# Performance work log

Measured on AMD Instinct MI355X. Metric: run time of the kernel, lower is better.

The kernel has to match this reference:

```python
import jax, jax.numpy as jnp
import numpy as np
import math

N = 50000      # nodes (single node type 'mapping_var')
D = 128        # in_feats
R = 3          # relations
E = 800000     # edges per relation
OUT = 64
ALPHA = 0.5
BETA1 = math.log(2.0)    # log(lambda/layer + 1), layer=1, lambda=1
BETA2 = math.log(1.5)    # layer=2
SLOPE = 0.01             # leaky_relu default negative slope


def setup_inputs() -> dict:
    key = jax.random.key(0)
    ks = jax.random.split(key, 8)
    x = jax.random.normal(ks[0], (N, D), dtype=jnp.float32)
    src = jax.random.randint(ks[1], (R, E), 0, N, dtype=jnp.int32)
    dst = jax.random.randint(ks[2], (R, E), 0, N, dtype=jnp.int32)
    W1 = jax.random.normal(ks[3], (R, D, D), dtype=jnp.float32) * 0.05
    b1 = jnp.zeros((R, D), dtype=jnp.float32)
    W2 = jax.random.normal(ks[4], (R, D, D), dtype=jnp.float32) * 0.05
    b2 = jnp.zeros((R, D), dtype=jnp.float32)
    Wlin = jax.random.normal(ks[5], (D, OUT), dtype=jnp.float32) * 0.05
    blin = jnp.zeros((OUT,), dtype=jnp.float32)
    return {"x": x, "src": src, "dst": dst, "W1": W1, "b1": b1,
            "W2": W2, "b2": b2, "Wlin": Wlin, "blin": blin}


def _gcn2_rel(h, feat0, src, dst, W, b, beta, act):
    """One GCN2Conv on one relation. h,feat0: [N,D]; src,dst: [E]."""
    ones = jnp.ones(src.shape, h.dtype)
    deg_out = jnp.maximum(jax.ops.segment_sum(ones, src, num_segments=N), 1.0)
    deg_in = jnp.maximum(jax.ops.segment_sum(ones, dst, num_segments=N), 1.0)
    hs = h * (deg_out ** -0.5)[:, None]              # src-side normalize
    agg = jax.ops.segment_sum(hs[src], dst, num_segments=N)  # SpMM via gather+scatter
    feat = agg * (deg_in ** -0.5)[:, None]           # dst-side normalize
    rst = feat * (1.0 - ALPHA) + ALPHA * feat0       # initial-residual blend
    rst = (1.0 - beta) * rst + beta * (rst @ W) + b  # identity mapping (project_initial_features)
    if act:
        rst = jnp.where(rst >= 0, rst, SLOPE * rst)  # leaky_relu
    return rst


def reference(x, src, dst, W1, b1, W2, b2, Wlin, blin):
    # conv1: per-relation GCN2Conv(layer=1, leaky_relu), mean-aggregate over relations
    h1 = jax.vmap(lambda s, d, w, bb: _gcn2_rel(x, x, s, d, w, bb, BETA1, True))(
        src, dst, W1, b1).mean(axis=0)
    # dropout: eval-mode identity
    # conv2: per-relation GCN2Conv(layer=2, no activation), feat_0 = original inputs
    h2 = jax.vmap(lambda s, d, w, bb: _gcn2_rel(h1, x, s, d, w, bb, BETA2, False))(
        src, dst, W2, b2).mean(axis=0)
    return h2 @ Wlin + blin
```

## Files before the change

kernel.cpp:

```cpp
#include <hip/hip_runtime.h>

#define NN    50000
#define DD    128
#define RR    3
#define EE    800000
#define OUTD  64
#define BKT   128
#define NBK   391
#define CAP   2560
#define CAPB  2560
#define CHUNK 8192
#define NCH   98
#define NPB   3125
#define SETUPB 6250
#define ALPHA_ 0.5f
#define SLOPE_ 0.01f
#define BETA1_ 0.6931471805599453f
#define BETA2_ 0.4054651081081644f

typedef __attribute__((ext_vector_type(8))) short short8;
typedef __attribute__((ext_vector_type(4))) float f32x4;

__device__ __forceinline__ unsigned short f2b(float f) {
    unsigned int u = __builtin_bit_cast(unsigned int, f);
    u += 0x7FFFu + ((u >> 16) & 1u);
    return (unsigned short)(u >> 16);
}
__device__ __forceinline__ unsigned int pack2(float lo, float hi) {
    return (unsigned int)f2b(lo) | ((unsigned int)f2b(hi) << 16);
}
__device__ __forceinline__ float blo(unsigned int w) { return __builtin_bit_cast(float, w << 16); }
__device__ __forceinline__ float bhi(unsigned int w) { return __builtin_bit_cast(float, w & 0xFFFF0000u); }

__global__ __launch_bounds__(256) void bin_kernel(
    const int* __restrict__ src, const int* __restrict__ dst,
    int* __restrict__ bcnt_d, int* __restrict__ bcnt_s,
    int* __restrict__ pairs_d, unsigned short* __restrict__ pairs_s)
{
    __shared__ int hist[NBK];
    __shared__ int lbase[NBK];
    __shared__ int gdelta[NBK];
    __shared__ int lcur[NBK];
    __shared__ unsigned int staging[CHUNK];
    unsigned short* staging16 = (unsigned short*)staging;
    const int tid = threadIdx.x;
    const int blk = blockIdx.x;
    const int phase = (blk >= RR * NCH);
    const int rb = phase ? blk - RR * NCH : blk;
    const int r = rb / NCH;
    const int chunk = rb % NCH;
    const int e0 = chunk * CHUNK;
    const int n = min(CHUNK, EE - e0);
    const int* sp = src + (size_t)r * EE + e0;
    const int* dp = dst + (size_t)r * EE + e0;
    const int* kp = phase ? sp : dp;

    for (int i = tid; i < NBK; i += 256) hist[i] = 0;
    __syncthreads();
    for (int i = tid; i < n; i += 256)
        atomicAdd(&hist[kp[i] >> 7], 1);
    __syncthreads();
    if (tid < 64) {
        int carry = 0;
        for (int c0 = 0; c0 < NBK; c0 += 64) {
            const int idx = c0 + tid;
            const int v = (idx < NBK) ? hist[idx] : 0;
            int incl = v;
            #pragma unroll
            for (int d = 1; d < 64; d <<= 1) {
                const int t = __shfl_up(incl, d, 64);
                if (tid >= d) incl += t;
            }
            if (idx < NBK) lbase[idx] = carry + incl - v;
            carry += __shfl(incl, 63, 64);
        }
    }
    __syncthreads();
    if (!phase) {
        for (int b = tid; b < NBK; b += 256) {
            lcur[b] = lbase[b];
            const int h = hist[b];
            if (h > 0) {
                const int gstart = (r * NBK + b) * CAP + atomicAdd(&bcnt_d[r * NBK + b], h);
                gdelta[b] = gstart - lbase[b];
            }
        }
        __syncthreads();
        for (int i = tid; i < n; i += 256) {
            const int d = dp[i];
            const int b = d >> 7;
            const int pos = atomicAdd(&lcur[b], 1);
            staging[pos] = (unsigned int)sp[i] | ((unsigned int)(d & 127) << 16)
                         | ((unsigned int)b << 23);
        }
        __syncthreads();
        for (int j = tid; j < n; j += 256) {
            const unsigned int v = staging[j];
            const int b = v >> 23;
            const int gi = gdelta[b] + j;
            const int lo = gi - (r * NBK + b) * CAP;
            if (lo < CAP) pairs_d[gi] = (int)(v & 0x7FFFFF);
        }
    } else {
        for (int b = tid; b < NBK; b += 256) {
            lcur[b] = lbase[b];
            const int h = hist[b];
            if (h > 0) {
                const int gstart = (r * NBK + b) * CAPB + atomicAdd(&bcnt_s[r * NBK + b], h);
                gdelta[b] = gstart - lbase[b];
            }
        }
        __syncthreads();
        for (int i = tid; i < n; i += 256) {
            const int s = sp[i];
            const int b = s >> 7;
            const int pos = atomicAdd(&lcur[b], 1);
            staging16[pos] = (unsigned short)((b << 7) | (s & 127));
        }
        __syncthreads();
        for (int j = tid; j < n; j += 256) {
            const unsigned short v = staging16[j];
            const int b = v >> 7;
            const int gi = gdelta[b] + j;
            const int lo = gi - (r * NBK + b) * CAPB;
            if (lo < CAPB) pairs_s[gi] = v;
        }
    }
}

__global__ __launch_bounds__(256) void dego_setup_kernel(
    const unsigned short* __restrict__ pairs_s, const int* __restrict__ bcnt_s,
    float* __restrict__ dego_r,
    const float* __restrict__ x, unsigned short* __restrict__ xb,
    const float* __restrict__ W1, const float* __restrict__ W2,
    const float* __restrict__ Wlin, unsigned short* __restrict__ Wt1,
    unsigned short* __restrict__ Wt2, unsigned short* __restrict__ WlT)
{
    __shared__ int scnt[BKT];
    const int tid = threadIdx.x;
    const int blk = blockIdx.x;
    if (blk < RR * NBK) {
        const int n2 = min(bcnt_s[blk], CAPB);
        const unsigned short* ps = pairs_s + (size_t)blk * CAPB;
        if (tid < BKT) scnt[tid] = 0;
        __syncthreads();
        for (int i = tid; i < n2; i += 256)
            atomicAdd(&scnt[ps[i] & 127], 1);
        __syncthreads();
        if (tid < BKT) {
            const int r = blk / NBK;
            const int g = (blk % NBK) * BKT + tid;
            if (g < NN)
                dego_r[r * NN + g] = rsqrtf((float)max(scnt[tid], 1));
        }
    } else {
        const int i = (blk - RR * NBK) * 256 + tid;
        {
            const float4 v = ((const float4*)x)[i];
            ushort4 o;
            o.x = f2b(v.x); o.y = f2b(v.y); o.z = f2b(v.z); o.w = f2b(v.w);
            ((ushort4*)xb)[i] = o;
        }
        if (i < RR * DD * DD) {
            const int r = i >> 14, rem = i & 16383, nn = rem >> 7, k = rem & 127;
            const float diag = (k == nn) ? 1.0f : 0.0f;
            const float w1 = W1[r * DD * DD + k * DD + nn];
            Wt1[i] = f2b(BETA1_ * w1 + diag * (1.0f - BETA1_));
            const float w2 = W2[r * DD * DD + k * DD + nn];
            Wt2[i] = f2b((BETA2_ * w2 + diag * (1.0f - BETA2_)) * (1.0f / 3.0f));
        } else if (i < RR * DD * DD + OUTD * DD) {
            const int j = i - RR * DD * DD;
            const int nn = j >> 7, k = j & 127;
            WlT[j] = f2b(Wlin[k * OUTD + nn]);
        }
    }
}

__global__ __launch_bounds__(256) void sort_kernel(
    int* __restrict__ pairs_d, const int* __restrict__ bcnt_d,
    const float* __restrict__ dego_r,
    int* __restrict__ off_g, int* __restrict__ cnt_g, float* __restrict__ degi_r)
{
    __shared__ int stage[CAP];
    __shared__ int cnt[BKT];
    __shared__ int base[BKT];
    __shared__ int pos[BKT];
    const int tid = threadIdx.x;
    const int bid = blockIdx.x;
    const int rr = bid / NBK;
    const int n = min(bcnt_d[bid], CAP);
    int* pp = pairs_d + (size_t)bid * CAP;
    const float* dego = dego_r + (size_t)rr * NN;
    if (tid < BKT) cnt[tid] = 0;
    __syncthreads();
    for (int i = tid; i < n; i += 256) {
        const int p = pp[i];
        stage[i] = p;
        atomicAdd(&cnt[p >> 16], 1);
    }
    __syncthreads();
    if (tid < 64) {
        int carry = 0;
        for (int c0 = 0; c0 < BKT; c0 += 64) {
            const int v = cnt[c0 + tid];
            int incl = v;
            #pragma unroll
            for (int d = 1; d < 64; d <<= 1) {
                const int t = __shfl_up(incl, d, 64);
                if (tid >= d) incl += t;
            }
            base[c0 + tid] = carry + incl - v;
            carry += __shfl(incl, 63, 64);
        }
    }
    __syncthreads();
    if (tid < BKT) {
        pos[tid] = base[tid];
        const int g = (bid % NBK) * BKT + tid;
        if (g < NN) {
            off_g[rr * NN + g] = bid * CAP + base[tid];
            cnt_g[rr * NN + g] = cnt[tid];
            degi_r[rr * NN + g] = rsqrtf((float)max(cnt[tid], 1));
        }
    }
    __syncthreads();
    for (int i = tid; i < n; i += 256) {
        const int p = stage[i];
        const int q = atomicAdd(&pos[p >> 16], 1);
        const int s = p & 0xFFFF;
        pp[q] = s | ((int)f2b(dego[s]) << 16);
    }
}

__global__ __launch_bounds__(256) void pull_all_kernel(
    const unsigned short* __restrict__ hb,
    const unsigned short* __restrict__ xb,
    const int* __restrict__ csrw, const int* __restrict__ off_g,
    const int* __restrict__ cnt_g, const float* __restrict__ degi_r,
    unsigned short* __restrict__ aggb)
{
    const int blk = blockIdx.x;
    const int r = blk / NPB;
    const int node = (blk % NPB) * 16 + (threadIdx.x >> 4);
    const int lane = threadIdx.x & 15;
    const int gi = r * NN + node;
    const int j0 = off_g[gi];
    const int j1 = j0 + cnt_g[gi];
    const uint4* hb4 = (const uint4*)hb;
    float a0 = 0.f, a1 = 0.f, a2 = 0.f, a3 = 0.f, a4 = 0.f, a5 = 0.f, a6 = 0.f, a7 = 0.f;
    int j = j0;
    for (; j + 4 <= j1; j += 4) {
        const unsigned int p0 = csrw[j],     p1 = csrw[j + 1];
        const unsigned int p2 = csrw[j + 2], p3 = csrw[j + 3];
        const float n0 = bhi(p0), n1 = bhi(p1), n2 = bhi(p2), n3 = bhi(p3);
        const uint4 q0 = hb4[(size_t)(p0 & 0xFFFF) * 16 + lane];
        const uint4 q1 = hb4[(size_t)(p1 & 0xFFFF) * 16 + lane];
        const uint4 q2 = hb4[(size_t)(p2 & 0xFFFF) * 16 + lane];
        const uint4 q3 = hb4[(size_t)(p3 & 0xFFFF) * 16 + lane];
        a0 += blo(q0.x) * n0 + blo(q1.x) * n1 + blo(q2.x) * n2 + blo(q3.x) * n3;
        a1 += bhi(q0.x) * n0 + bhi(q1.x) * n1 + bhi(q2.x) * n2 + bhi(q3.x) * n3;
        a2 += blo(q0.y) * n0 + blo(q1.y) * n1 + blo(q2.y) * n2 + blo(q3.y) * n3;
        a3 += bhi(q0.y) * n0 + bhi(q1.y) * n1 + bhi(q2.y) * n2 + bhi(q3.y) * n3;
        a4 += blo(q0.z) * n0 + blo(q1.z) * n1 + blo(q2.z) * n2 + blo(q3.z) * n3;
        a5 += bhi(q0.z) * n0 + bhi(q1.z) * n1 + bhi(q2.z) * n2 + bhi(q3.z) * n3;
        a6 += blo(q0.w) * n0 + blo(q1.w) * n1 + blo(q2.w) * n2 + blo(q3.w) * n3;
        a7 += bhi(q0.w) * n0 + bhi(q1.w) * n1 + bhi(q2.w) * n2 + bhi(q3.w) * n3;
    }
    for (; j < j1; ++j) {
        const unsigned int p0 = csrw[j];
        const float n0 = bhi(p0);
        const uint4 q0 = hb4[(size_t)(p0 & 0xFFFF) * 16 + lane];
        a0 += blo(q0.x) * n0; a1 += bhi(q0.x) * n0;
        a2 += blo(q0.y) * n0; a3 += bhi(q0.y) * n0;
        a4 += blo(q0.z) * n0; a5 += bhi(q0.z) * n0;
        a6 += blo(q0.w) * n0; a7 += bhi(q0.w) * n0;
    }
    const float nd = degi_r[gi] * (1.0f - ALPHA_);
    const uint4 xq = ((const uint4*)xb)[(size_t)node * 16 + lane];
    uint4 o;
    o.x = pack2(a0 * nd + ALPHA_ * blo(xq.x), a1 * nd + ALPHA_ * bhi(xq.x));
    o.y = pack2(a2 * nd + ALPHA_ * blo(xq.y), a3 * nd + ALPHA_ * bhi(xq.y));
    o.z = pack2(a4 * nd + ALPHA_ * blo(xq.z), a5 * nd + ALPHA_ * bhi(xq.z));
    o.w = pack2(a6 * nd + ALPHA_ * blo(xq.w), a7 * nd + ALPHA_ * bhi(xq.w));
    ((uint4*)aggb)[(size_t)gi * 16 + lane] = o;
}

template<int LIN>
__global__ __launch_bounds__(256) void conv_mfma_kernel(
    const unsigned short* __restrict__ aggb,
    const unsigned short* __restrict__ WtG,
    const float* __restrict__ bias,
    const unsigned short* __restrict__ WlT,
    const float* __restrict__ blin,
    unsigned short* __restrict__ houtb,
    float* __restrict__ outf)
{
    __shared__ unsigned short WtL[DD * 136];
    uint4* WtL4 = (uint4*)WtL;
    const int tid  = threadIdx.x;
    const int wave = tid >> 6;
    const int lane = tid & 63;
    const int l15  = lane & 15;
    const int q    = lane >> 4;
    const int blockRow = blockIdx.x * 64;
    const int row0 = blockRow + wave * 16;
    const int arow = min(row0 + l15, NN - 1);

    f32x4 o[8];
    if (LIN) {
        #pragma unroll
        for (int ct = 0; ct < 8; ++ct) {
            const int col = ct * 16 + l15;
            const float bv = (bias[col] + bias[DD + col] + bias[2 * DD + col]) * (1.0f / 3.0f);
            o[ct] = (f32x4){bv, bv, bv, bv};
        }
    } else {
        #pragma unroll
        for (int ct = 0; ct < 8; ++ct) o[ct] = (f32x4){0.f, 0.f, 0.f, 0.f};
    }

    short8 a_cur[4], a_nxt[4];
    {
        const uint4* ap = (const uint4*)aggb + (size_t)arow * 16 + q;
        #pragma unroll
        for (int ks = 0; ks < 4; ++ks)
            a_cur[ks] = __builtin_bit_cast(short8, ap[ks * 4]);
    }

    for (int r = 0; r < RR; ++r) {
        __syncthreads();
        const uint4* wg = (const uint4*)(WtG + (size_t)r * DD * DD);
        for (int i = tid; i < DD * 16; i += 256)
            WtL4[(i >> 4) * 17 + (i & 15)] = wg[i];
        if (r + 1 < RR) {
            const uint4* ap = (const uint4*)aggb + ((size_t)(r + 1) * NN + arow) * 16 + q;
            #pragma unroll
            for (int ks = 0; ks < 4; ++ks)
                a_nxt[ks] = __builtin_bit_cast(short8, ap[ks * 4]);
        }
        __syncthreads();

        #pragma unroll
        for (int ct = 0; ct < 8; ++ct) {
            f32x4 acc;
            if (LIN) {
                acc = o[ct];
            } else {
                const float bv = bias[r * DD + ct * 16 + l15];
                acc = (f32x4){bv, bv, bv, bv};
            }
            const int nrow = ct * 16 + l15;
            #pragma unroll
            for (int ks = 0; ks < 4; ++ks) {
                const short8 b = __builtin_bit_cast(short8, WtL4[nrow * 17 + ks * 4 + q]);
                acc = __builtin_amdgcn_mfma_f32_16x16x32_bf16(a_cur[ks], b, acc, 0, 0, 0);
            }
            if (LIN) {
                o[ct] = acc;
            } else {
                #pragma unroll
                for (int e = 0; e < 4; ++e) {
                    float v = acc[e];
                    v = v >= 0.f ? v : SLOPE_ * v;
                    o[ct][e] += v * (1.0f / 3.0f);
                }
            }
        }
        #pragma unroll
        for (int ks = 0; ks < 4; ++ks) a_cur[ks] = a_nxt[ks];
    }

    __syncthreads();
    unsigned short* tile = WtL;
    #pragma unroll
    for (int ct = 0; ct < 8; ++ct) {
        const int col = ct * 16 + l15;
        #pragma unroll
        for (int e = 0; e < 4; ++e) {
            const int lrow = wave * 16 + q * 4 + e;
            tile[lrow * 136 + col] = f2b(o[ct][e]);
        }
    }
    if (LIN) {
        uint4* wl4 = WtL4 + 64 * 17;
        const uint4* wg = (const uint4*)WlT;
        for (int i = tid; i < OUTD * 16; i += 256)
            wl4[(i >> 4) * 17 + (i & 15)] = wg[i];
    }
    __syncthreads();

    if (!LIN) {
        for (int i = tid; i < 64 * 16; i += 256) {
            const int lrow = i >> 4, c = i & 15;
            const int grow = blockRow + lrow;
            if (grow < NN)
                ((uint4*)houtb)[(size_t)grow * 16 + c] = WtL4[lrow * 17 + c];
        }
    } else {
        short8 a2[4];
        const int lrow = wave * 16 + l15;
        #pragma unroll
        for (int ks = 0; ks < 4; ++ks)
            a2[ks] = __builtin_bit_cast(short8, WtL4[lrow * 17 + ks * 4 + q]);
        #pragma unroll
        for (int ct = 0; ct < 4; ++ct) {
            const int col = ct * 16 + l15;
            const float bv = blin[col];
            f32x4 acc = (f32x4){bv, bv, bv, bv};
            #pragma unroll
            for (int ks = 0; ks < 4; ++ks) {
                const short8 b = __builtin_bit_cast(short8, WtL4[(64 + col) * 17 + ks * 4 + q]);
                acc = __builtin_amdgcn_mfma_f32_16x16x32_bf16(a2[ks], b, acc, 0, 0, 0);
            }
            #pragma unroll
            for (int e = 0; e < 4; ++e) {
                const int grow = row0 + q * 4 + e;
                if (grow < NN) outf[(size_t)grow * OUTD + col] = acc[e];
            }
        }
    }
}

extern "C" void kernel_launch(void* const* d_in, const int* in_sizes, int n_in,
                              void* d_out, int out_size, void* d_ws, size_t ws_size,
                              hipStream_t stream)
{
    const float* x    = (const float*)d_in[0];
    const int*   src  = (const int*)  d_in[1];
    const int*   dst  = (const int*)  d_in[2];
    const float* W1   = (const float*)d_in[3];
    const float* b1   = (const float*)d_in[4];
    const float* W2   = (const float*)d_in[5];
    const float* b2   = (const float*)d_in[6];
    const float* Wlin = (const float*)d_in[7];
    const float* blin = (const float*)d_in[8];
    float* out = (float*)d_out;

    int*   bcnt_d  = (int*)d_ws;
    int*   bcnt_s  = bcnt_d + RR * NBK;
    float* dego_r  = (float*)(bcnt_s + RR * NBK);
    float* degi_r  = dego_r + RR * NN;
    int*   off_g   = (int*)(degi_r + RR * NN);
    int*   cnt_g   = off_g + RR * NN;
    int*   pairs_d = cnt_g + RR * NN + 2;
    unsigned short* pairs_s = (unsigned short*)(pairs_d + (size_t)RR * NBK * CAP);
    unsigned short* xb   = pairs_s + (size_t)RR * NBK * CAPB;
    unsigned short* h1b  = xb + (size_t)NN * DD;
    unsigned short* aggb = h1b + (size_t)NN * DD;
    unsigned short* Wt1  = aggb + (size_t)RR * NN * DD;
    unsigned short* Wt2  = Wt1 + RR * DD * DD;
    unsigned short* WlT  = Wt2 + RR * DD * DD;

    hipMemsetAsync(bcnt_d, 0, (size_t)2 * RR * NBK * sizeof(int), stream);

    const int gemm_blocks = (NN + 63) / 64;

    bin_kernel<<<2 * RR * NCH, 256, 0, stream>>>(src, dst, bcnt_d, bcnt_s, pairs_d, pairs_s);
    dego_setup_kernel<<<RR * NBK + SETUPB, 256, 0, stream>>>(
        pairs_s, bcnt_s, dego_r, x, xb, W1, W2, Wlin, Wt1, Wt2, WlT);
    sort_kernel<<<RR * NBK, 256, 0, stream>>>(
        pairs_d, bcnt_d, dego_r, off_g, cnt_g, degi_r);

    pull_all_kernel<<<RR * NPB, 256, 0, stream>>>(
        xb, xb, pairs_d, off_g, cnt_g, degi_r, aggb);
    conv_mfma_kernel<0><<<gemm_blocks, 256, 0, stream>>>(
        aggb, Wt1, b1, nullptr, nullptr, h1b, nullptr);

    pull_all_kernel<<<RR * NPB, 256, 0, stream>>>(
        h1b, xb, pairs_d, off_g, cnt_g, degi_r, aggb);
    conv_mfma_kernel<1><<<gemm_blocks, 256, 0, stream>>>(
        aggb, Wt2, b2, WlT, blin, nullptr, out);
}
```

Baseline: 405.7 us.

## Fold layer-2 projection and final linear into pre-aggregation 64-wide GEMM

Layer 2 had no activation, so its per-relation identity mapping, the relation mean and the final linear are folded into combined matrices M_r = (beta*W2_r + (1-beta)I)·Wlin/3, plus a constant bias vector. These are built in the setup kernel. A new GEMM projects h1 (and x for the residual term) to 64 columns before aggregation, and a 64-wide pull kernel then gathers and sums over the three relations straight into the output. This halves the gathered bytes in the second SpMM and removes the 128x128 second conv GEMM, at the cost of an extra bf16 rounding of the projected features and a small serial matmul in setup.

```diff
diff --git a/kernel.cpp b/kernel.cpp
--- a/kernel.cpp
+++ b/kernel.cpp
@@ -13,6 +13,9 @@
 #define NCH   98
 #define NPB   3125
 #define SETUPB 6250
+#define MCB   49
+#define PGB   391
+#define P64B  3125
 #define ALPHA_ 0.5f
 #define SLOPE_ 0.01f
 #define BETA1_ 0.6931471805599453f
@@ -20,6 +23,7 @@
 
 typedef __attribute__((ext_vector_type(8))) short short8;
 typedef __attribute__((ext_vector_type(4))) float f32x4;
+typedef __attribute__((ext_vector_type(4))) unsigned int u32x4;
 
 __device__ __forceinline__ unsigned short f2b(float f) {
     unsigned int u = __builtin_bit_cast(unsigned int, f);
@@ -134,7 +138,9 @@
     const float* __restrict__ x, unsigned short* __restrict__ xb,
     const float* __restrict__ W1, const float* __restrict__ W2,
     const float* __restrict__ Wlin, unsigned short* __restrict__ Wt1,
-    unsigned short* __restrict__ Wt2, unsigned short* __restrict__ WlT)
+    unsigned short* __restrict__ Wt2, unsigned short* __restrict__ WlT,
+    const float* __restrict__ b2, const float* __restrict__ blin,
+    unsigned short* __restrict__ MT, float* __restrict__ Cbuf)
 {
     __shared__ int scnt[BKT];
     const int tid = threadIdx.x;
@@ -153,7 +159,7 @@
             if (g < NN)
                 dego_r[r * NN + g] = rsqrtf((float)max(scnt[tid], 1));
         }
-    } else {
+    } else if (blk < RR * NBK + SETUPB) {
         const int i = (blk - RR * NBK) * 256 + tid;
         {
             const float4 v = ((const float4*)x)[i];
@@ -173,6 +179,31 @@
             const int nn = j >> 7, k = j & 127;
             WlT[j] = f2b(Wlin[k * OUTD + nn]);
         }
+    } else {
+        const int mb = blk - RR * NBK - SETUPB;
+        if (mb < MCB - 1) {
+            const int base = (mb * 256 + tid) * 2;
+            #pragma unroll
+            for (int ii = 0; ii < 2; ++ii) {
+                const int gidx = base + ii;
+                const int r = gidx >> 13;
+                const int rem = gidx & 8191;
+                const int o = rem >> 7, k = rem & 127;
+                float s = 0.f;
+                for (int nn = 0; nn < DD; ++nn)
+                    s += W2[r * DD * DD + k * DD + nn] * Wlin[nn * OUTD + o];
+                MT[gidx] = f2b((BETA2_ / 3.0f) * s + ((1.0f - BETA2_) / 3.0f) * Wlin[k * OUTD + o]);
+            }
+        } else {
+            if (tid < OUTD) {
+                float s = blin[tid];
+                for (int nn = 0; nn < DD; ++nn) {
+                    const float mb2 = (b2[nn] + b2[DD + nn] + b2[2 * DD + nn]) * (1.0f / 3.0f);
+                    s += mb2 * Wlin[nn * OUTD + tid];
+                }
+                Cbuf[tid] = s;
+            }
+        }
     }
 }
 
@@ -246,17 +277,17 @@
     const int gi = r * NN + node;
     const int j0 = off_g[gi];
     const int j1 = j0 + cnt_g[gi];
-    const uint4* hb4 = (const uint4*)hb;
+    const u32x4* hb4 = (const u32x4*)hb;
     float a0 = 0.f, a1 = 0.f, a2 = 0.f, a3 = 0.f, a4 = 0.f, a5 = 0.f, a6 = 0.f, a7 = 0.f;
     int j = j0;
     for (; j + 4 <= j1; j += 4) {
         const unsigned int p0 = csrw[j],     p1 = csrw[j + 1];
         const unsigned int p2 = csrw[j + 2], p3 = csrw[j + 3];
         const float n0 = bhi(p0), n1 = bhi(p1), n2 = bhi(p2), n3 = bhi(p3);
-        const uint4 q0 = hb4[(size_t)(p0 & 0xFFFF) * 16 + lane];
-        const uint4 q1 = hb4[(size_t)(p1 & 0xFFFF) * 16 + lane];
-        const uint4 q2 = hb4[(size_t)(p2 & 0xFFFF) * 16 + lane];
-        const uint4 q3 = hb4[(size_t)(p3 & 0xFFFF) * 16 + lane];
+        const u32x4 q0 = hb4[(size_t)(p0 & 0xFFFF) * 16 + lane];
+        const u32x4 q1 = hb4[(size_t)(p1 & 0xFFFF) * 16 + lane];
+        const u32x4 q2 = hb4[(size_t)(p2 & 0xFFFF) * 16 + lane];
+        const u32x4 q3 = hb4[(size_t)(p3 & 0xFFFF) * 16 + lane];
         a0 += blo(q0.x) * n0 + blo(q1.x) * n1 + blo(q2.x) * n2 + blo(q3.x) * n3;
         a1 += bhi(q0.x) * n0 + bhi(q1.x) * n1 + bhi(q2.x) * n2 + bhi(q3.x) * n3;
         a2 += blo(q0.y) * n0 + blo(q1.y) * n1 + blo(q2.y) * n2 + blo(q3.y) * n3;
@@ -269,20 +300,20 @@
     for (; j < j1; ++j) {
         const unsigned int p0 = csrw[j];
         const float n0 = bhi(p0);
-        const uint4 q0 = hb4[(size_t)(p0 & 0xFFFF) * 16 + lane];
+        const u32x4 q0 = hb4[(size_t)(p0 & 0xFFFF) * 16 + lane];
         a0 += blo(q0.x) * n0; a1 += bhi(q0.x) * n0;
         a2 += blo(q0.y) * n0; a3 += bhi(q0.y) * n0;
         a4 += blo(q0.z) * n0; a5 += bhi(q0.z) * n0;
         a6 += blo(q0.w) * n0; a7 += bhi(q0.w) * n0;
     }
     const float nd = degi_r[gi] * (1.0f - ALPHA_);
-    const uint4 xq = ((const uint4*)xb)[(size_t)node * 16 + lane];
-    uint4 o;
+    const u32x4 xq = ((const u32x4*)xb)[(size_t)node * 16 + lane];
+    u32x4 o;
     o.x = pack2(a0 * nd + ALPHA_ * blo(xq.x), a1 * nd + ALPHA_ * bhi(xq.x));
     o.y = pack2(a2 * nd + ALPHA_ * blo(xq.y), a3 * nd + ALPHA_ * bhi(xq.y));
     o.z = pack2(a4 * nd + ALPHA_ * blo(xq.z), a5 * nd + ALPHA_ * bhi(xq.z));
     o.w = pack2(a6 * nd + ALPHA_ * blo(xq.w), a7 * nd + ALPHA_ * bhi(xq.w));
-    ((uint4*)aggb)[(size_t)gi * 16 + lane] = o;
+    ((u32x4*)aggb)[(size_t)gi * 16 + lane] = o;
 }
 
 template<int LIN>
@@ -381,44 +412,138 @@
             tile[lrow * 136 + col] = f2b(o[ct][e]);
         }
     }
-    if (LIN) {
-        uint4* wl4 = WtL4 + 64 * 17;
-        const uint4* wg = (const uint4*)WlT;
-        for (int i = tid; i < OUTD * 16; i += 256)
-            wl4[(i >> 4) * 17 + (i & 15)] = wg[i];
-    }
-    __syncthreads();
-
-    if (!LIN) {
-        for (int i = tid; i < 64 * 16; i += 256) {
-            const int lrow = i >> 4, c = i & 15;
-            const int grow = blockRow + lrow;
-            if (grow < NN)
-                ((uint4*)houtb)[(size_t)grow * 16 + c] = WtL4[lrow * 17 + c];
-        }
-    } else {
-        short8 a2[4];
-        const int lrow = wave * 16 + l15;
-        #pragma unroll
-        for (int ks = 0; ks < 4; ++ks)
-            a2[ks] = __builtin_bit_cast(short8, WtL4[lrow * 17 + ks * 4 + q]);
+    __syncthreads();
+    for (int i = tid; i < 64 * 16; i += 256) {
+        const int lrow = i >> 4, c = i & 15;
+        const int grow = blockRow + lrow;
+        if (grow < NN)
+            ((uint4*)houtb)[(size_t)grow * 16 + c] = WtL4[lrow * 17 + c];
+    }
+}
+
+__global__ __launch_bounds__(512) void pgemm_kernel(
+    const unsigned short* __restrict__ h1b,
+    const unsigned short* __restrict__ xb,
+    const unsigned short* __restrict__ MT,
+    unsigned short* __restrict__ Pb,
+    unsigned short* __restrict__ Qb)
+{
+    __shared__ unsigned short MTL[RR * 64 * 136];
+    uint4* MTL4 = (uint4*)MTL;
+    const int tid  = threadIdx.x;
+    const int wave = tid >> 6;
+    const int lane = tid & 63;
+    const int l15  = lane & 15;
+    const int q    = lane >> 4;
+    const int blockRow = blockIdx.x * 128;
+    const int row0 = blockRow + wave * 16;
+    const int arow = min(row0 + l15, NN - 1);
+
+    {
+        const uint4* mg = (const uint4*)MT;
+        for (int i = tid; i < RR * 64 * 16; i += 512)
+            MTL4[(i >> 4) * 17 + (i & 15)] = mg[i];
+    }
+    short8 ah[4], ax[4];
+    {
+        const uint4* hp = (const uint4*)h1b + (size_t)arow * 16 + q;
+        const uint4* xp = (const uint4*)xb + (size_t)arow * 16 + q;
+        #pragma unroll
+        for (int ks = 0; ks < 4; ++ks) {
+            ah[ks] = __builtin_bit_cast(short8, hp[ks * 4]);
+            ax[ks] = __builtin_bit_cast(short8, xp[ks * 4]);
+        }
+    }
+    __syncthreads();
+
+    for (int r = 0; r < RR; ++r) {
         #pragma unroll
         for (int ct = 0; ct < 4; ++ct) {
-            const int col = ct * 16 + l15;
-            const float bv = blin[col];
-            f32x4 acc = (f32x4){bv, bv, bv, bv};
+            f32x4 acc = (f32x4){0.f, 0.f, 0.f, 0.f};
+            const int orow = r * 64 + ct * 16 + l15;
             #pragma unroll
             for (int ks = 0; ks < 4; ++ks) {
-                const short8 b = __builtin_bit_cast(short8, WtL4[(64 + col) * 17 + ks * 4 + q]);
-                acc = __builtin_amdgcn_mfma_f32_16x16x32_bf16(a2[ks], b, acc, 0, 0, 0);
+                const short8 b = __builtin_bit_cast(short8, MTL4[orow * 17 + ks * 4 + q]);
+                acc = __builtin_amdgcn_mfma_f32_16x16x32_bf16(ah[ks], b, acc, 0, 0, 0);
             }
             #pragma unroll
             for (int e = 0; e < 4; ++e) {
                 const int grow = row0 + q * 4 + e;
-                if (grow < NN) outf[(size_t)grow * OUTD + col] = acc[e];
-            }
-        }
-    }
+                if (grow < NN)
+                    Pb[((size_t)r * NN + grow) * OUTD + ct * 16 + l15] = f2b(acc[e]);
+            }
+        }
+    }
+    #pragma unroll
+    for (int ct = 0; ct < 4; ++ct) {
+        f32x4 acc = (f32x4){0.f, 0.f, 0.f, 0.f};
+        for (int r = 0; r < RR; ++r) {
+            const int orow = r * 64 + ct * 16 + l15;
+            #pragma unroll
+            for (int ks = 0; ks < 4; ++ks) {
+                const short8 b = __builtin_bit_cast(short8, MTL4[orow * 17 + ks * 4 + q]);
+                acc = __builtin_amdgcn_mfma_f32_16x16x32_bf16(ax[ks], b, acc, 0, 0, 0);
+            }
+        }
+        #pragma unroll
+        for (int e = 0; e < 4; ++e) {
+            const int grow = row0 + q * 4 + e;
+            if (grow < NN)
+                Qb[(size_t)grow * OUTD + ct * 16 + l15] = f2b(acc[e] * ALPHA_);
+        }
+    }
+}
+
+__global__ __launch_bounds__(256) void pull64_kernel(
+    const unsigned short* __restrict__ Pb,
+    const unsigned short* __restrict__ Qb,
+    const float* __restrict__ Cbuf,
+    const int* __restrict__ csrw, const int* __restrict__ off_g,
+    const int* __restrict__ cnt_g, const float* __restrict__ degi_r,
+    float* __restrict__ outf)
+{
+    const int node = blockIdx.x * 16 + (threadIdx.x >> 4);
+    const int lane = threadIdx.x & 15;
+    const uint2* P2 = (const uint2*)Pb;
+    float t0, t1, t2, t3;
+    {
+        const uint2 qq = ((const uint2*)Qb)[(size_t)node * 16 + lane];
+        const float4 cv = ((const float4*)Cbuf)[lane];
+        t0 = blo(qq.x) + cv.x; t1 = bhi(qq.x) + cv.y;
+        t2 = blo(qq.y) + cv.z; t3 = bhi(qq.y) + cv.w;
+    }
+    for (int r = 0; r < RR; ++r) {
+        const int gi = r * NN + node;
+        const int j0 = off_g[gi];
+        const int j1 = j0 + cnt_g[gi];
+        const uint2* Pr = P2 + (size_t)r * NN * 16;
+        float a0 = 0.f, a1 = 0.f, a2 = 0.f, a3 = 0.f;
+        int j = j0;
+        for (; j + 4 <= j1; j += 4) {
+            const unsigned int p0 = csrw[j],     p1 = csrw[j + 1];
+            const unsigned int p2 = csrw[j + 2], p3 = csrw[j + 3];
+            const float n0 = bhi(p0), n1 = bhi(p1), n2 = bhi(p2), n3 = bhi(p3);
+            const uint2 q0 = Pr[(size_t)(p0 & 0xFFFF) * 16 + lane];
+            const uint2 q1 = Pr[(size_t)(p1 & 0xFFFF) * 16 + lane];
+            const uint2 q2 = Pr[(size_t)(p2 & 0xFFFF) * 16 + lane];
+            const uint2 q3 = Pr[(size_t)(p3 & 0xFFFF) * 16 + lane];
+            a0 += blo(q0.x) * n0 + blo(q1.x) * n1 + blo(q2.x) * n2 + blo(q3.x) * n3;
+            a1 += bhi(q0.x) * n0 + bhi(q1.x) * n1 + bhi(q2.x) * n2 + bhi(q3.x) * n3;
+            a2 += blo(q0.y) * n0 + blo(q1.y) * n1 + blo(q2.y) * n2 + blo(q3.y) * n3;
+            a3 += bhi(q0.y) * n0 + bhi(q1.y) * n1 + bhi(q2.y) * n2 + bhi(q3.y) * n3;
+        }
+        for (; j < j1; ++j) {
+            const unsigned int p0 = csrw[j];
+            const float n0 = bhi(p0);
+            const uint2 q0 = Pr[(size_t)(p0 & 0xFFFF) * 16 + lane];
+            a0 += blo(q0.x) * n0; a1 += bhi(q0.x) * n0;
+            a2 += blo(q0.y) * n0; a3 += bhi(q0.y) * n0;
+        }
+        const float nd = degi_r[gi] * (1.0f - ALPHA_);
+        t0 += a0 * nd; t1 += a1 * nd; t2 += a2 * nd; t3 += a3 * nd;
+    }
+    float4 ov; ov.x = t0; ov.y = t1; ov.z = t2; ov.w = t3;
+    ((float4*)outf)[(size_t)node * 16 + lane] = ov;
 }
 
 extern "C" void kernel_launch(void* const* d_in, const int* in_sizes, int n_in,
@@ -450,14 +575,18 @@
     unsigned short* Wt1  = aggb + (size_t)RR * NN * DD;
     unsigned short* Wt2  = Wt1 + RR * DD * DD;
     unsigned short* WlT  = Wt2 + RR * DD * DD;
+    unsigned short* MT   = WlT + OUTD * DD;
+    float*          Cbuf = (float*)(MT + RR * DD * OUTD);
+    unsigned short* Pb = aggb;
+    unsigned short* Qb = aggb + (size_t)RR * NN * OUTD;
 
     hipMemsetAsync(bcnt_d, 0, (size_t)2 * RR * NBK * sizeof(int), stream);
 
     const int gemm_blocks = (NN + 63) / 64;
 
     bin_kernel<<<2 * RR * NCH, 256, 0, stream>>>(src, dst, bcnt_d, bcnt_s, pairs_d, pairs_s);
-    dego_setup_kernel<<<RR * NBK + SETUPB, 256, 0, stream>>>(
-        pairs_s, bcnt_s, dego_r, x, xb, W1, W2, Wlin, Wt1, Wt2, WlT);
+    dego_setup_kernel<<<RR * NBK + SETUPB + MCB, 256, 0, stream>>>(
+        pairs_s, bcnt_s, dego_r, x, xb, W1, W2, Wlin, Wt1, Wt2, WlT, b2, blin, MT, Cbuf);
     sort_kernel<<<RR * NBK, 256, 0, stream>>>(
         pairs_d, bcnt_d, dego_r, off_g, cnt_g, degi_r);
 
@@ -466,8 +595,7 @@
     conv_mfma_kernel<0><<<gemm_blocks, 256, 0, stream>>>(
         aggb, Wt1, b1, nullptr, nullptr, h1b, nullptr);
 
-    pull_all_kernel<<<RR * NPB, 256, 0, stream>>>(
-        h1b, xb, pairs_d, off_g, cnt_g, degi_r, aggb);
-    conv_mfma_kernel<1><<<gemm_blocks, 256, 0, stream>>>(
-        aggb, Wt2, b2, WlT, blin, nullptr, out);
-}
+    pgemm_kernel<<<PGB, 512, 0, stream>>>(h1b, xb, MT, Pb, Qb);
+    pull64_kernel<<<P64B, 256, 0, stream>>>(
+        Pb, Qb, Cbuf, pairs_d, off_g, cnt_g, degi_r, out);
+}
```

After: 376.5 us, median of 2. 1.08x faster.
